# Optimization experiments

Measured on AMD Instinct MI355X. Metric: run time of the kernel, lower is better.

The kernel has to match this reference:

```python
import jax, jax.numpy as jnp
import numpy as np

N = 50000
E = 1600000
IN_CH = 128
HID = 16
HEADS = 8
OUT_CH = 1
NEG_SLOPE = 0.2


def setup_inputs() -> dict:
    key = jax.random.key(0)
    ks = jax.random.split(key, 12)
    x = jax.random.normal(ks[0], (N, IN_CH), dtype=jnp.float32)
    edge_index = jax.random.randint(ks[1], (2, E), 0, N, dtype=jnp.int64)
    s1 = 1.0 / np.sqrt(IN_CH)
    s2 = 1.0 / np.sqrt(HEADS * HID)
    W1 = jax.random.normal(ks[2], (IN_CH, HEADS * HID), dtype=jnp.float32) * s1
    att_src1 = jax.random.normal(ks[3], (HEADS, HID), dtype=jnp.float32) * s1
    att_dst1 = jax.random.normal(ks[4], (HEADS, HID), dtype=jnp.float32) * s1
    b1 = jnp.zeros((HEADS * HID,), dtype=jnp.float32)
    W2 = jax.random.normal(ks[5], (HEADS * HID, OUT_CH), dtype=jnp.float32) * s2
    att_src2 = jax.random.normal(ks[6], (1, OUT_CH), dtype=jnp.float32) * s2
    att_dst2 = jax.random.normal(ks[7], (1, OUT_CH), dtype=jnp.float32) * s2
    b2 = jnp.zeros((OUT_CH,), dtype=jnp.float32)
    return {"x": x, "edge_index": edge_index,
            "W1": W1, "att_src1": att_src1, "att_dst1": att_dst1, "b1": b1,
            "W2": W2, "att_src2": att_src2, "att_dst2": att_dst2, "b2": b2}


def gat_conv(x, src, dst, W, att_src, att_dst, b, heads, concat):
    n = x.shape[0]
    h = (x @ W).reshape(n, heads, -1)               # [N, H, C]
    a_s = jnp.einsum('nhc,hc->nh', h, att_src)      # [N, H]
    a_d = jnp.einsum('nhc,hc->nh', h, att_dst)
    e = jax.nn.leaky_relu(a_s[src] + a_d[dst], NEG_SLOPE)  # [E, H]
    # segment softmax over incoming edges of each dst node
    emax = jax.ops.segment_max(e, dst, num_segments=n)
    p = jnp.exp(e - emax[dst])
    denom = jax.ops.segment_sum(p, dst, num_segments=n)
    alpha = p / (denom[dst] + 1e-16)                 # [E, H]
    msg = h[src] * alpha[:, :, None]                 # [E, H, C]
    out = jax.ops.segment_sum(msg, dst, num_segments=n)  # [N, H, C]
    if concat:
        out = out.reshape(n, -1)
    else:
        out = out.mean(axis=1)
    return out + b


def reference(x, edge_index, W1, att_src1, att_dst1, b1, W2, att_src2, att_dst2, b2):
    n = x.shape[0]
    loops = jnp.arange(n, dtype=edge_index.dtype)
    src = jnp.concatenate([edge_index[0], loops])    # PyG add_self_loops=True
    dst = jnp.concatenate([edge_index[1], loops])
    h = gat_conv(x, src, dst, W1, att_src1, att_dst1, b1, HEADS, True)
    h = jax.nn.elu(h)
    out = gat_conv(h, src, dst, W2, att_src2, att_dst2, b2, 1, False)
    return out
```

## Files before the change

kernel.cpp:

```cpp
#include <hip/hip_runtime.h>
#include <hip/hip_fp16.h>
#include <math.h>

#define N_NODES 50000
#define N_EDGES 1600000
#define NEG 0.2f

#define PB 256
#define CHUNK ((N_EDGES + PB - 1) / PB)
#define BSHIFT 6
#define NBUCK ((N_NODES + 63) >> BSHIFT)
#define LDSE 2816


__global__ __launch_bounds__(1024) void count_pass(const int* __restrict__ ei, int* __restrict__ counts) {
    __shared__ int h[NBUCK];
    for (int i = threadIdx.x; i < NBUCK; i += 1024) h[i] = 0;
    __syncthreads();
    int p = blockIdx.x;
    int e0 = p * CHUNK, e1 = min(e0 + CHUNK, N_EDGES);
    for (int e = e0 + threadIdx.x; e < e1; e += 1024) {
        int d = ei[N_EDGES + e];
        atomicAdd(&h[d >> BSHIFT], 1);
    }
    __syncthreads();
    for (int i = threadIdx.x; i < NBUCK; i += 1024) counts[p * NBUCK + i] = h[i];
}

__global__ __launch_bounds__(256) void scan_blocks(const int* __restrict__ counts,
                                                   int* __restrict__ starts, int* __restrict__ btot) {
    __shared__ int s[256];
    int b = blockIdx.x;
    int t = threadIdx.x;
    int v = counts[t * NBUCK + b];
    s[t] = v;
    __syncthreads();
    for (int off = 1; off < 256; off <<= 1) {
        int u = (t >= off) ? s[t - off] : 0;
        __syncthreads();
        s[t] += u;
        __syncthreads();
    }
    starts[t * NBUCK + b] = s[t] - v;
    if (t == 255) btot[b] = s[255];
}

__global__ __launch_bounds__(1024) void scan_total(const int* __restrict__ btot, int* __restrict__ bbase) {
    __shared__ int s[1024];
    int t = threadIdx.x;
    int v = (t < NBUCK) ? btot[t] : 0;
    s[t] = v;
    __syncthreads();
    for (int off = 1; off < 1024; off <<= 1) {
        int x = (t >= off) ? s[t - off] : 0;
        __syncthreads();
        s[t] += x;
        __syncthreads();
    }
    if (t < NBUCK) bbase[t] = s[t] - v;
    if (t == 0) bbase[NBUCK] = N_EDGES;
}

__global__ __launch_bounds__(1024) void bin_scatter(const int* __restrict__ ei, const int* __restrict__ starts,
                                                    const int* __restrict__ bbase, int* __restrict__ temp) {
    __shared__ int cur[NBUCK];
    int p = blockIdx.x;
    for (int i = threadIdx.x; i < NBUCK; i += 1024)
        cur[i] = bbase[i] + starts[p * NBUCK + i];
    __syncthreads();
    int e0 = p * CHUNK, e1 = min(e0 + CHUNK, N_EDGES);
    for (int e = e0 + threadIdx.x; e < e1; e += 1024) {
        int s = ei[e];
        int d = ei[N_EDGES + e];
        int b = d >> BSHIFT;
        int pos = atomicAdd(&cur[b], 1);
        temp[pos] = s | ((d & 63) << 16);
    }
}


__global__ __launch_bounds__(256) void gemm1_kernel(const float* __restrict__ x, const float* __restrict__ W1,
                                                    const float* __restrict__ att_s, const float* __restrict__ att_d,
                                                    __half2* __restrict__ h1, float* __restrict__ as1,
                                                    float* __restrict__ ad1) {
    __shared__ float xs[128][36];
    int n0 = blockIdx.x * 32;
    int t = threadIdx.x;
#pragma unroll
    for (int i = 0; i < 16; ++i) {
        int f = i * 256 + t;
        int r = f >> 7, c = f & 127;
        int gr = n0 + r;
        float v = (gr < N_NODES) ? x[(size_t)gr * 128 + c] : 0.f;
        xs[c][r] = v;
    }
    __syncthreads();
    int c0 = (t & 31) * 4;
    int r0 = (t >> 5) * 4;
    float acc[4][4];
#pragma unroll
    for (int i = 0; i < 4; ++i)
#pragma unroll
        for (int j = 0; j < 4; ++j) acc[i][j] = 0.f;
#pragma unroll 4
    for (int k = 0; k < 128; ++k) {
        float4 w = *(const float4*)(W1 + k * 128 + c0);
        float4 xr = *(const float4*)(&xs[k][r0]);
        float xv[4] = {xr.x, xr.y, xr.z, xr.w};
        float wv[4] = {w.x, w.y, w.z, w.w};
#pragma unroll
        for (int i = 0; i < 4; ++i)
#pragma unroll
            for (int j = 0; j < 4; ++j) acc[i][j] += xv[i] * wv[j];
    }
#pragma unroll
    for (int i = 0; i < 4; ++i) {
        int row = n0 + r0 + i;
        if (row < N_NODES) {
            __half2 p0 = __float22half2_rn(make_float2(acc[i][0], acc[i][1]));
            __half2 p1 = __float22half2_rn(make_float2(acc[i][2], acc[i][3]));
            h1[(size_t)row * 64 + (c0 >> 1)] = p0;
            h1[(size_t)row * 64 + (c0 >> 1) + 1] = p1;
        }
    }
    int head = (t & 31) >> 2;
    float ps[4], pd[4];
#pragma unroll
    for (int i = 0; i < 4; ++i) {
        float s = 0.f, d = 0.f;
#pragma unroll
        for (int j = 0; j < 4; ++j) {
            s += acc[i][j] * att_s[c0 + j];
            d += acc[i][j] * att_d[c0 + j];
        }
        ps[i] = s; pd[i] = d;
    }
#pragma unroll
    for (int i = 0; i < 4; ++i) {
        ps[i] += __shfl_xor(ps[i], 1, 64);
        ps[i] += __shfl_xor(ps[i], 2, 64);
        pd[i] += __shfl_xor(pd[i], 1, 64);
        pd[i] += __shfl_xor(pd[i], 2, 64);
    }
    if ((t & 3) == 0) {
#pragma unroll
        for (int i = 0; i < 4; ++i) {
            int row = n0 + r0 + i;
            if (row < N_NODES) {
                as1[row * 8 + head] = ps[i];
                ad1[row * 8 + head] = pd[i];
            }
        }
    }
}


__device__ __forceinline__ float lrelu(float v) { return fmaxf(v, NEG * v); }

__global__ __launch_bounds__(512) void agg1_kernel(const char* __restrict__ h1c, const char* __restrict__ as1c,
                                                   const float* __restrict__ ad1, const int* __restrict__ temp,
                                                   const int* __restrict__ bbase, const float* __restrict__ b1,
                                                   const float* __restrict__ W2, float* __restrict__ h2out) {
    __shared__ int lsrc[LDSE];
    __shared__ int cnt[64];
    __shared__ int cur[64];
    __shared__ int lrp[64];
    int b = blockIdx.x, t = threadIdx.x;
    int base = bbase[b];
    int nE = bbase[b + 1] - base;
    if (t < 64) cnt[t] = 0;
    __syncthreads();
    for (int i = t; i < nE; i += 512)
        atomicAdd(&cnt[(unsigned)temp[base + i] >> 16], 1);
    __syncthreads();
    if (t < 64) {
        int v = cnt[t];
        int incl = v;
#pragma unroll
        for (int off = 1; off < 64; off <<= 1) {
            int u = __shfl_up(incl, off, 64);
            if (t >= off) incl += u;
        }
        int excl = incl - v;
        lrp[t] = excl;
        cur[t] = excl;
    }
    __syncthreads();
    for (int i = t; i < nE; i += 512) {
        int v = temp[base + i];
        int pos = atomicAdd(&cur[(unsigned)v >> 16], 1);
        lsrc[pos] = v & 0xFFFF;
    }
    __syncthreads();

    int lane = t & 63;
    int wave = t >> 6;
    int hB = lane >> 3;
    int hP = lane & 7;
    unsigned lane4 = (unsigned)lane << 2;
    unsigned hP4 = (unsigned)hP << 2;
    int bperm_base = hB << 2;
    int prod = lane >> 3;

    for (int kk = 0; kk < 8; ++kk) {
        int k = wave * 8 + kk;
        int n = b * 64 + k;
        if (n >= N_NODES) continue;

        float adP = ad1[n * 8 + hP];
        float adC = ad1[n * 8 + hB];
        float asC = *(const float*)(as1c + ((unsigned)n * 32u + ((unsigned)hB << 2)));
        float p_self = __expf(lrelu(asC + adC));
        __half2 hvs = *(const __half2*)(h1c + (((unsigned)n << 8) + lane4));
        float acc0 = p_self * __half2float(__low2half(hvs));
        float acc1 = p_self * __half2float(__high2half(hvs));
        float l = p_self;

        int jb = lrp[k];
        int deg = cnt[k];
        int j = 0;
        for (; j + 8 <= deg; j += 8) {
            int sP = lsrc[jb + j + prod];
            float aP = *(const float*)(as1c + (((unsigned)sP << 5) + hP4));
            float pP = __expf(lrelu(aP + adP));
            int pPi = __float_as_int(pP);
#pragma unroll
            for (int e = 0; e < 8; ++e) {
                int addr = bperm_base + e * 32;
                float p = __int_as_float(__builtin_amdgcn_ds_bpermute(addr, pPi));
                int s = __builtin_amdgcn_ds_bpermute(addr, sP);
                __half2 hv = *(const __half2*)(h1c + (((unsigned)s << 8) + lane4));
                acc0 += p * __half2float(__low2half(hv));
                acc1 += p * __half2float(__high2half(hv));
                l += p;
            }
        }
        if (j < deg) {
            int r = deg - j;
            int sP = 0;
            float pP = 0.f;
            if (j + prod < deg) {
                sP = lsrc[jb + j + prod];
                float aP = *(const float*)(as1c + (((unsigned)sP << 5) + hP4));
                pP = __expf(lrelu(aP + adP));
            }
            int pPi = __float_as_int(pP);
            for (int e = 0; e < r; ++e) {
                int addr = bperm_base + e * 32;
                float p = __int_as_float(__builtin_amdgcn_ds_bpermute(addr, pPi));
                int s = __builtin_amdgcn_ds_bpermute(addr, sP);
                __half2 hv = *(const __half2*)(h1c + (((unsigned)s << 8) + lane4));
                acc0 += p * __half2float(__low2half(hv));
                acc1 += p * __half2float(__high2half(hv));
                l += p;
            }
        }

        float inv = 1.f / (l + 1e-16f);
        int c0 = lane * 2;
        float y0 = acc0 * inv + b1[c0];
        float y1 = acc1 * inv + b1[c0 + 1];
        y0 = y0 > 0.f ? y0 : expm1f(y0);
        y1 = y1 > 0.f ? y1 : expm1f(y1);
        float part = y0 * W2[c0] + y1 * W2[c0 + 1];
#pragma unroll
        for (int off = 32; off; off >>= 1) part += __shfl_down(part, off, 64);
        if (lane == 0) h2out[n] = part;
    }
}


__global__ __launch_bounds__(256) void agg2_kernel(const float* __restrict__ h2, const int* __restrict__ temp,
                                                   const int* __restrict__ bbase, const float* __restrict__ att_s2,
                                                   const float* __restrict__ att_d2, const float* __restrict__ b2,
                                                   float* __restrict__ out) {
    __shared__ int lsrc[LDSE];
    __shared__ int cnt[64];
    __shared__ int cur[64];
    __shared__ int lrp[64];
    int b = blockIdx.x, t = threadIdx.x;
    int base = bbase[b];
    int nE = bbase[b + 1] - base;
    if (t < 64) cnt[t] = 0;
    __syncthreads();
    for (int i = t; i < nE; i += 256)
        atomicAdd(&cnt[(unsigned)temp[base + i] >> 16], 1);
    __syncthreads();
    if (t < 64) {
        int v = cnt[t];
        int incl = v;
#pragma unroll
        for (int off = 1; off < 64; off <<= 1) {
            int u = __shfl_up(incl, off, 64);
            if (t >= off) incl += u;
        }
        int excl = incl - v;
        lrp[t] = excl;
        cur[t] = excl;
    }
    __syncthreads();
    for (int i = t; i < nE; i += 256) {
        int v = temp[base + i];
        int pos = atomicAdd(&cur[(unsigned)v >> 16], 1);
        lsrc[pos] = v & 0xFFFF;
    }
    __syncthreads();

    float asw = att_s2[0], adw = att_d2[0];
    int lane = t & 63;
    int wave = t >> 6;
    int sub = lane & 7;
    int grp = lane >> 3;
    for (int round = 0; round < 2; ++round) {
        int k = wave * 16 + round * 8 + grp;
        int n = b * 64 + k;
        float acc = 0.f, l = 0.f;
        if (n < N_NODES) {
            float h2n = h2[n];
            float ad = h2n * adw;
            if (sub == 0) {
                float p = __expf(lrelu(h2n * asw + ad));
                acc = p * h2n;
                l = p;
            }
            int jb = lrp[k];
            int deg = cnt[k];
            for (int jj = sub; jj < deg; jj += 8) {
                int s = lsrc[jb + jj];
                float hs = h2[s];
                float p = __expf(lrelu(hs * asw + ad));
                acc += p * hs;
                l += p;
            }
#pragma unroll
            for (int off = 4; off; off >>= 1) {
                acc += __shfl_down(acc, off, 8);
                l += __shfl_down(l, off, 8);
            }
            if (sub == 0) out[n] = acc / (l + 1e-16f) + b2[0];
        }
    }
}


extern "C" void kernel_launch(void* const* d_in, const int* in_sizes, int n_in,
                              void* d_out, int out_size, void* d_ws, size_t ws_size,
                              hipStream_t stream) {
    const float* x = (const float*)d_in[0];
    const int* ei = (const int*)d_in[1];
    const float* W1 = (const float*)d_in[2];
    const float* att_s1 = (const float*)d_in[3];
    const float* att_d1 = (const float*)d_in[4];
    const float* b1 = (const float*)d_in[5];
    const float* W2 = (const float*)d_in[6];
    const float* att_s2 = (const float*)d_in[7];
    const float* att_d2 = (const float*)d_in[8];
    const float* b2 = (const float*)d_in[9];
    float* out = (float*)d_out;

    char* p = (char*)d_ws;
    auto alloc = [&](size_t bytes) {
        char* q = p;
        p += (bytes + 255) & ~(size_t)255;
        return q;
    };
    int* counts = (int*)alloc((size_t)PB * NBUCK * 4);
    int* starts = (int*)alloc((size_t)PB * NBUCK * 4);
    int* btot = (int*)alloc((size_t)NBUCK * 4);
    int* bbase = (int*)alloc((size_t)(NBUCK + 1) * 4);
    int* temp = (int*)alloc((size_t)N_EDGES * 4);
    __half2* h1 = (__half2*)alloc((size_t)N_NODES * 128 * 2);
    float* as1 = (float*)alloc((size_t)N_NODES * 8 * 4);
    float* ad1 = (float*)alloc((size_t)N_NODES * 8 * 4);
    float* h2 = (float*)alloc((size_t)N_NODES * 4);

    count_pass<<<PB, 1024, 0, stream>>>(ei, counts);
    scan_blocks<<<NBUCK, 256, 0, stream>>>(counts, starts, btot);
    scan_total<<<1, 1024, 0, stream>>>(btot, bbase);
    bin_scatter<<<PB, 1024, 0, stream>>>(ei, starts, bbase, temp);
    gemm1_kernel<<<(N_NODES + 31) / 32, 256, 0, stream>>>(x, W1, att_s1, att_d1, h1, as1, ad1);
    agg1_kernel<<<NBUCK, 512, 0, stream>>>((const char*)h1, (const char*)as1, ad1, temp, bbase, b1, W2, h2);
    agg2_kernel<<<NBUCK, 256, 0, stream>>>(h2, temp, bbase, att_s2, att_d2, b2, out);
}
```

Measured before the change: 234.6 us.

## Fuse preprocessing kernels and merge edge scatter with GEMM launch

Bucket totals are now accumulated with global atomics in count_pass, which lets the per-bucket scan and the total scan share a single launch; block NBUCK of that launch scans the bucket totals. The edge binning scatter and the first-layer GEMM are merged into one heterogeneous launch that uses a shared-memory union, so the two independent jobs can run concurrently. agg1 is changed to 256 threads, with each wave handling 16 nodes instead of 8. This cuts the launch count and lets the GEMM overlap the scatter, at the cost of an extra memset and a scatter that now runs with 256-thread blocks instead of 1024.

```diff
diff --git a/kernel.cpp b/kernel.cpp
--- a/kernel.cpp
+++ b/kernel.cpp
@@ -11,9 +11,11 @@
 #define BSHIFT 6
 #define NBUCK ((N_NODES + 63) >> BSHIFT)
 #define LDSE 2816
-
-
-__global__ __launch_bounds__(1024) void count_pass(const int* __restrict__ ei, int* __restrict__ counts) {
+#define GEMMB ((N_NODES + 31) / 32)
+
+
+__global__ __launch_bounds__(1024) void count_pass(const int* __restrict__ ei, int* __restrict__ counts,
+                                                   int* __restrict__ btot) {
     __shared__ int h[NBUCK];
     for (int i = threadIdx.x; i < NBUCK; i += 1024) h[i] = 0;
     __syncthreads();
@@ -24,75 +26,93 @@
         atomicAdd(&h[d >> BSHIFT], 1);
     }
     __syncthreads();
-    for (int i = threadIdx.x; i < NBUCK; i += 1024) counts[p * NBUCK + i] = h[i];
-}
-
-__global__ __launch_bounds__(256) void scan_blocks(const int* __restrict__ counts,
-                                                   int* __restrict__ starts, int* __restrict__ btot) {
+    for (int i = threadIdx.x; i < NBUCK; i += 1024) {
+        counts[p * NBUCK + i] = h[i];
+        if (h[i]) atomicAdd(&btot[i], h[i]);
+    }
+}
+
+
+__global__ __launch_bounds__(256) void scan_fused(const int* __restrict__ counts, const int* __restrict__ btot,
+                                                  int* __restrict__ starts, int* __restrict__ bbase) {
     __shared__ int s[256];
     int b = blockIdx.x;
     int t = threadIdx.x;
-    int v = counts[t * NBUCK + b];
-    s[t] = v;
-    __syncthreads();
-    for (int off = 1; off < 256; off <<= 1) {
-        int u = (t >= off) ? s[t - off] : 0;
+    if (b < NBUCK) {
+        int v = counts[t * NBUCK + b];
+        s[t] = v;
         __syncthreads();
-        s[t] += u;
+        for (int off = 1; off < 256; off <<= 1) {
+            int u = (t >= off) ? s[t - off] : 0;
+            __syncthreads();
+            s[t] += u;
+            __syncthreads();
+        }
+        starts[t * NBUCK + b] = s[t] - v;
+    } else {
+        int base = t * 4;
+        int c[4];
+        int sum = 0;
+#pragma unroll
+        for (int k = 0; k < 4; ++k) {
+            c[k] = (base + k < NBUCK) ? btot[base + k] : 0;
+            sum += c[k];
+        }
+        s[t] = sum;
         __syncthreads();
-    }
-    starts[t * NBUCK + b] = s[t] - v;
-    if (t == 255) btot[b] = s[255];
-}
-
-__global__ __launch_bounds__(1024) void scan_total(const int* __restrict__ btot, int* __restrict__ bbase) {
-    __shared__ int s[1024];
-    int t = threadIdx.x;
-    int v = (t < NBUCK) ? btot[t] : 0;
-    s[t] = v;
-    __syncthreads();
-    for (int off = 1; off < 1024; off <<= 1) {
-        int x = (t >= off) ? s[t - off] : 0;
-        __syncthreads();
-        s[t] += x;
-        __syncthreads();
-    }
-    if (t < NBUCK) bbase[t] = s[t] - v;
-    if (t == 0) bbase[NBUCK] = N_EDGES;
-}
-
-__global__ __launch_bounds__(1024) void bin_scatter(const int* __restrict__ ei, const int* __restrict__ starts,
-                                                    const int* __restrict__ bbase, int* __restrict__ temp) {
-    __shared__ int cur[NBUCK];
-    int p = blockIdx.x;
-    for (int i = threadIdx.x; i < NBUCK; i += 1024)
-        cur[i] = bbase[i] + starts[p * NBUCK + i];
-    __syncthreads();
-    int e0 = p * CHUNK, e1 = min(e0 + CHUNK, N_EDGES);
-    for (int e = e0 + threadIdx.x; e < e1; e += 1024) {
-        int s = ei[e];
-        int d = ei[N_EDGES + e];
-        int b = d >> BSHIFT;
-        int pos = atomicAdd(&cur[b], 1);
-        temp[pos] = s | ((d & 63) << 16);
-    }
-}
-
-
-__global__ __launch_bounds__(256) void gemm1_kernel(const float* __restrict__ x, const float* __restrict__ W1,
+        for (int off = 1; off < 256; off <<= 1) {
+            int u = (t >= off) ? s[t - off] : 0;
+            __syncthreads();
+            s[t] += u;
+            __syncthreads();
+        }
+        int run = s[t] - sum;
+#pragma unroll
+        for (int k = 0; k < 4; ++k) {
+            if (base + k < NBUCK) {
+                bbase[base + k] = run;
+                run += c[k];
+            }
+        }
+        if (t == 0) bbase[NBUCK] = N_EDGES;
+    }
+}
+
+
+__global__ __launch_bounds__(256) void scatter_gemm(const int* __restrict__ ei, const int* __restrict__ starts,
+                                                    const int* __restrict__ bbase, int* __restrict__ temp,
+                                                    const float* __restrict__ x, const float* __restrict__ W1,
                                                     const float* __restrict__ att_s, const float* __restrict__ att_d,
                                                     __half2* __restrict__ h1, float* __restrict__ as1,
                                                     float* __restrict__ ad1) {
-    __shared__ float xs[128][36];
-    int n0 = blockIdx.x * 32;
+    __shared__ union {
+        float xs[128][36];
+        int cur[NBUCK];
+    } u;
     int t = threadIdx.x;
+    if (blockIdx.x < PB) {
+        int p = blockIdx.x;
+        for (int i = t; i < NBUCK; i += 256)
+            u.cur[i] = bbase[i] + starts[p * NBUCK + i];
+        __syncthreads();
+        int e0 = p * CHUNK, e1 = min(e0 + CHUNK, N_EDGES);
+        for (int e = e0 + t; e < e1; e += 256) {
+            int s = ei[e];
+            int d = ei[N_EDGES + e];
+            int b = d >> BSHIFT;
+            int pos = atomicAdd(&u.cur[b], 1);
+            temp[pos] = s | ((d & 63) << 16);
+        }
+        return;
+    }
+    int n0 = (blockIdx.x - PB) * 32;
 #pragma unroll
     for (int i = 0; i < 16; ++i) {
         int f = i * 256 + t;
         int r = f >> 7, c = f & 127;
         int gr = n0 + r;
         float v = (gr < N_NODES) ? x[(size_t)gr * 128 + c] : 0.f;
-        xs[c][r] = v;
+        u.xs[c][r] = v;
     }
     __syncthreads();
     int c0 = (t & 31) * 4;
@@ -105,7 +125,7 @@
 #pragma unroll 4
     for (int k = 0; k < 128; ++k) {
         float4 w = *(const float4*)(W1 + k * 128 + c0);
-        float4 xr = *(const float4*)(&xs[k][r0]);
+        float4 xr = *(const float4*)(&u.xs[k][r0]);
         float xv[4] = {xr.x, xr.y, xr.z, xr.w};
         float wv[4] = {w.x, w.y, w.z, w.w};
 #pragma unroll
@@ -157,7 +177,7 @@
 
 __device__ __forceinline__ float lrelu(float v) { return fmaxf(v, NEG * v); }
 
-__global__ __launch_bounds__(512) void agg1_kernel(const char* __restrict__ h1c, const char* __restrict__ as1c,
+__global__ __launch_bounds__(256) void agg1_kernel(const char* __restrict__ h1c, const char* __restrict__ as1c,
                                                    const float* __restrict__ ad1, const int* __restrict__ temp,
                                                    const int* __restrict__ bbase, const float* __restrict__ b1,
                                                    const float* __restrict__ W2, float* __restrict__ h2out) {
@@ -170,7 +190,7 @@
     int nE = bbase[b + 1] - base;
     if (t < 64) cnt[t] = 0;
     __syncthreads();
-    for (int i = t; i < nE; i += 512)
+    for (int i = t; i < nE; i += 256)
         atomicAdd(&cnt[(unsigned)temp[base + i] >> 16], 1);
     __syncthreads();
     if (t < 64) {
@@ -186,7 +206,7 @@
         cur[t] = excl;
     }
     __syncthreads();
-    for (int i = t; i < nE; i += 512) {
+    for (int i = t; i < nE; i += 256) {
         int v = temp[base + i];
         int pos = atomicAdd(&cur[(unsigned)v >> 16], 1);
         lsrc[pos] = v & 0xFFFF;
@@ -202,8 +222,8 @@
     int bperm_base = hB << 2;
     int prod = lane >> 3;
 
-    for (int kk = 0; kk < 8; ++kk) {
-        int k = wave * 8 + kk;
+    for (int kk = 0; kk < 16; ++kk) {
+        int k = wave * 16 + kk;
         int n = b * 64 + k;
         if (n >= N_NODES) continue;
 
@@ -374,11 +394,11 @@
     float* ad1 = (float*)alloc((size_t)N_NODES * 8 * 4);
     float* h2 = (float*)alloc((size_t)N_NODES * 4);
 
-    count_pass<<<PB, 1024, 0, stream>>>(ei, counts);
-    scan_blocks<<<NBUCK, 256, 0, stream>>>(counts, starts, btot);
-    scan_total<<<1, 1024, 0, stream>>>(btot, bbase);
-    bin_scatter<<<PB, 1024, 0, stream>>>(ei, starts, bbase, temp);
-    gemm1_kernel<<<(N_NODES + 31) / 32, 256, 0, stream>>>(x, W1, att_s1, att_d1, h1, as1, ad1);
-    agg1_kernel<<<NBUCK, 512, 0, stream>>>((const char*)h1, (const char*)as1, ad1, temp, bbase, b1, W2, h2);
+    hipMemsetAsync(btot, 0, (size_t)NBUCK * 4, stream);
+    count_pass<<<PB, 1024, 0, stream>>>(ei, counts, btot);
+    scan_fused<<<NBUCK + 1, 256, 0, stream>>>(counts, btot, starts, bbase);
+    scatter_gemm<<<PB + GEMMB, 256, 0, stream>>>(ei, starts, bbase, temp,
+                                                 x, W1, att_s1, att_d1, h1, as1, ad1);
+    agg1_kernel<<<NBUCK, 256, 0, stream>>>((const char*)h1, (const char*)as1, ad1, temp, bbase, b1, W2, h2);
     agg2_kernel<<<NBUCK, 256, 0, stream>>>(h2, temp, bbase, att_s2, att_d2, b2, out);
 }
```

Measured after the change: 258.6 us. 10.2% more time.

## Fuse bin scatter with GEMM launch and shrink buckets to 32 nodes

Applied to the files above, without the earlier changes.

Merges the edge bin-scatter and the first-layer GEMM into one launch, where the first PB blocks do the scatter and the rest do the GEMM. The two independent phases can then overlap and one launch is removed. Bucket size also drops from 64 to 32 nodes, which doubles the number of aggregation blocks and halves their thread count and LDS use. scan_total now handles two buckets per thread to cover the larger bucket count. The risk is an LDS overflow in a high-degree bucket (LDSE is 1536) and more atomics and count overhead from the extra buckets.

```diff
diff --git a/kernel.cpp b/kernel.cpp
--- a/kernel.cpp
+++ b/kernel.cpp
@@ -8,9 +8,10 @@
 
 #define PB 256
 #define CHUNK ((N_EDGES + PB - 1) / PB)
-#define BSHIFT 6
-#define NBUCK ((N_NODES + 63) >> BSHIFT)
-#define LDSE 2816
+#define BSHIFT 5
+#define NBUCK ((N_NODES + 31) >> BSHIFT)
+#define LDSE 1536
+#define GEMMB ((N_NODES + 31) / 32)
 
 
 __global__ __launch_bounds__(1024) void count_pass(const int* __restrict__ ei, int* __restrict__ counts) {
@@ -26,6 +27,7 @@
     __syncthreads();
     for (int i = threadIdx.x; i < NBUCK; i += 1024) counts[p * NBUCK + i] = h[i];
 }
+
 
 __global__ __launch_bounds__(256) void scan_blocks(const int* __restrict__ counts,
                                                    int* __restrict__ starts, int* __restrict__ btot) {
@@ -48,8 +50,11 @@
 __global__ __launch_bounds__(1024) void scan_total(const int* __restrict__ btot, int* __restrict__ bbase) {
     __shared__ int s[1024];
     int t = threadIdx.x;
-    int v = (t < NBUCK) ? btot[t] : 0;
-    s[t] = v;
+    int base = t * 2;
+    int c0 = (base < NBUCK) ? btot[base] : 0;
+    int c1 = (base + 1 < NBUCK) ? btot[base + 1] : 0;
+    int sum = c0 + c1;
+    s[t] = sum;
     __syncthreads();
     for (int off = 1; off < 1024; off <<= 1) {
         int x = (t >= off) ? s[t - off] : 0;
@@ -57,42 +62,47 @@
         s[t] += x;
         __syncthreads();
     }
-    if (t < NBUCK) bbase[t] = s[t] - v;
+    int run = s[t] - sum;
+    if (base < NBUCK) bbase[base] = run;
+    if (base + 1 < NBUCK) bbase[base + 1] = run + c0;
     if (t == 0) bbase[NBUCK] = N_EDGES;
 }
 
-__global__ __launch_bounds__(1024) void bin_scatter(const int* __restrict__ ei, const int* __restrict__ starts,
-                                                    const int* __restrict__ bbase, int* __restrict__ temp) {
-    __shared__ int cur[NBUCK];
-    int p = blockIdx.x;
-    for (int i = threadIdx.x; i < NBUCK; i += 1024)
-        cur[i] = bbase[i] + starts[p * NBUCK + i];
-    __syncthreads();
-    int e0 = p * CHUNK, e1 = min(e0 + CHUNK, N_EDGES);
-    for (int e = e0 + threadIdx.x; e < e1; e += 1024) {
-        int s = ei[e];
-        int d = ei[N_EDGES + e];
-        int b = d >> BSHIFT;
-        int pos = atomicAdd(&cur[b], 1);
-        temp[pos] = s | ((d & 63) << 16);
-    }
-}
-
-
-__global__ __launch_bounds__(256) void gemm1_kernel(const float* __restrict__ x, const float* __restrict__ W1,
+
+__global__ __launch_bounds__(256) void scatter_gemm(const int* __restrict__ ei, const int* __restrict__ starts,
+                                                    const int* __restrict__ bbase, int* __restrict__ temp,
+                                                    const float* __restrict__ x, const float* __restrict__ W1,
                                                     const float* __restrict__ att_s, const float* __restrict__ att_d,
                                                     __half2* __restrict__ h1, float* __restrict__ as1,
                                                     float* __restrict__ ad1) {
-    __shared__ float xs[128][36];
-    int n0 = blockIdx.x * 32;
+    __shared__ union {
+        float xs[128][36];
+        int cur[NBUCK];
+    } u;
     int t = threadIdx.x;
+    if (blockIdx.x < PB) {
+        int p = blockIdx.x;
+        for (int i = t; i < NBUCK; i += 256)
+            u.cur[i] = bbase[i] + starts[p * NBUCK + i];
+        __syncthreads();
+        int e0 = p * CHUNK, e1 = min(e0 + CHUNK, N_EDGES);
+        for (int e = e0 + t; e < e1; e += 256) {
+            int s = ei[e];
+            int d = ei[N_EDGES + e];
+            int b = d >> BSHIFT;
+            int pos = atomicAdd(&u.cur[b], 1);
+            temp[pos] = s | ((d & 31) << 16);
+        }
+        return;
+    }
+    int n0 = (blockIdx.x - PB) * 32;
 #pragma unroll
     for (int i = 0; i < 16; ++i) {
         int f = i * 256 + t;
         int r = f >> 7, c = f & 127;
         int gr = n0 + r;
         float v = (gr < N_NODES) ? x[(size_t)gr * 128 + c] : 0.f;
-        xs[c][r] = v;
+        u.xs[c][r] = v;
     }
     __syncthreads();
     int c0 = (t & 31) * 4;
@@ -105,7 +115,7 @@
 #pragma unroll 4
     for (int k = 0; k < 128; ++k) {
         float4 w = *(const float4*)(W1 + k * 128 + c0);
-        float4 xr = *(const float4*)(&xs[k][r0]);
+        float4 xr = *(const float4*)(&u.xs[k][r0]);
         float xv[4] = {xr.x, xr.y, xr.z, xr.w};
         float wv[4] = {w.x, w.y, w.z, w.w};
 #pragma unroll
@@ -157,28 +167,28 @@
 
 __device__ __forceinline__ float lrelu(float v) { return fmaxf(v, NEG * v); }
 
-__global__ __launch_bounds__(512) void agg1_kernel(const char* __restrict__ h1c, const char* __restrict__ as1c,
+__global__ __launch_bounds__(256) void agg1_kernel(const char* __restrict__ h1c, const char* __restrict__ as1c,
                                                    const float* __restrict__ ad1, const int* __restrict__ temp,
                                                    const int* __restrict__ bbase, const float* __restrict__ b1,
                                                    const float* __restrict__ W2, float* __restrict__ h2out) {
     __shared__ int lsrc[LDSE];
-    __shared__ int cnt[64];
-    __shared__ int cur[64];
-    __shared__ int lrp[64];
+    __shared__ int cnt[32];
+    __shared__ int cur[32];
+    __shared__ int lrp[32];
     int b = blockIdx.x, t = threadIdx.x;
     int base = bbase[b];
     int nE = bbase[b + 1] - base;
-    if (t < 64) cnt[t] = 0;
-    __syncthreads();
-    for (int i = t; i < nE; i += 512)
+    if (t < 32) cnt[t] = 0;
+    __syncthreads();
+    for (int i = t; i < nE; i += 256)
         atomicAdd(&cnt[(unsigned)temp[base + i] >> 16], 1);
     __syncthreads();
-    if (t < 64) {
+    if (t < 32) {
         int v = cnt[t];
         int incl = v;
 #pragma unroll
-        for (int off = 1; off < 64; off <<= 1) {
-            int u = __shfl_up(incl, off, 64);
+        for (int off = 1; off < 32; off <<= 1) {
+            int u = __shfl_up(incl, off, 32);
             if (t >= off) incl += u;
         }
         int excl = incl - v;
@@ -186,7 +196,7 @@
         cur[t] = excl;
     }
     __syncthreads();
-    for (int i = t; i < nE; i += 512) {
+    for (int i = t; i < nE; i += 256) {
         int v = temp[base + i];
         int pos = atomicAdd(&cur[(unsigned)v >> 16], 1);
         lsrc[pos] = v & 0xFFFF;
@@ -204,7 +214,7 @@
 
     for (int kk = 0; kk < 8; ++kk) {
         int k = wave * 8 + kk;
-        int n = b * 64 + k;
+        int n = b * 32 + k;
         if (n >= N_NODES) continue;
 
         float adP = ad1[n * 8 + hP];
@@ -275,23 +285,23 @@
                                                    const float* __restrict__ att_d2, const float* __restrict__ b2,
                                                    float* __restrict__ out) {
     __shared__ int lsrc[LDSE];
-    __shared__ int cnt[64];
-    __shared__ int cur[64];
-    __shared__ int lrp[64];
+    __shared__ int cnt[32];
+    __shared__ int cur[32];
+    __shared__ int lrp[32];
     int b = blockIdx.x, t = threadIdx.x;
     int base = bbase[b];
     int nE = bbase[b + 1] - base;
-    if (t < 64) cnt[t] = 0;
+    if (t < 32) cnt[t] = 0;
     __syncthreads();
     for (int i = t; i < nE; i += 256)
         atomicAdd(&cnt[(unsigned)temp[base + i] >> 16], 1);
     __syncthreads();
-    if (t < 64) {
+    if (t < 32) {
         int v = cnt[t];
         int incl = v;
 #pragma unroll
-        for (int off = 1; off < 64; off <<= 1) {
-            int u = __shfl_up(incl, off, 64);
+        for (int off = 1; off < 32; off <<= 1) {
+            int u = __shfl_up(incl, off, 32);
             if (t >= off) incl += u;
         }
         int excl = incl - v;
@@ -311,34 +321,32 @@
     int wave = t >> 6;
     int sub = lane & 7;
     int grp = lane >> 3;
-    for (int round = 0; round < 2; ++round) {
-        int k = wave * 16 + round * 8 + grp;
-        int n = b * 64 + k;
+    int k = wave * 8 + grp;
+    int n = b * 32 + k;
+    if (n < N_NODES) {
+        float h2n = h2[n];
+        float ad = h2n * adw;
         float acc = 0.f, l = 0.f;
-        if (n < N_NODES) {
-            float h2n = h2[n];
-            float ad = h2n * adw;
-            if (sub == 0) {
-                float p = __expf(lrelu(h2n * asw + ad));
-                acc = p * h2n;
-                l = p;
-            }
-            int jb = lrp[k];
-            int deg = cnt[k];
-            for (int jj = sub; jj < deg; jj += 8) {
-                int s = lsrc[jb + jj];
-                float hs = h2[s];
-                float p = __expf(lrelu(hs * asw + ad));
-                acc += p * hs;
-                l += p;
-            }
-#pragma unroll
-            for (int off = 4; off; off >>= 1) {
-                acc += __shfl_down(acc, off, 8);
-                l += __shfl_down(l, off, 8);
-            }
-            if (sub == 0) out[n] = acc / (l + 1e-16f) + b2[0];
-        }
+        if (sub == 0) {
+            float p = __expf(lrelu(h2n * asw + ad));
+            acc = p * h2n;
+            l = p;
+        }
+        int jb = lrp[k];
+        int deg = cnt[k];
+        for (int jj = sub; jj < deg; jj += 8) {
+            int s = lsrc[jb + jj];
+            float hs = h2[s];
+            float p = __expf(lrelu(hs * asw + ad));
+            acc += p * hs;
+            l += p;
+        }
+#pragma unroll
+        for (int off = 4; off; off >>= 1) {
+            acc += __shfl_down(acc, off, 8);
+            l += __shfl_down(l, off, 8);
+        }
+        if (sub == 0) out[n] = acc / (l + 1e-16f) + b2[0];
     }
 }
 
@@ -377,8 +385,8 @@
     count_pass<<<PB, 1024, 0, stream>>>(ei, counts);
     scan_blocks<<<NBUCK, 256, 0, stream>>>(counts, starts, btot);
     scan_total<<<1, 1024, 0, stream>>>(btot, bbase);
-    bin_scatter<<<PB, 1024, 0, stream>>>(ei, starts, bbase, temp);
-    gemm1_kernel<<<(N_NODES + 31) / 32, 256, 0, stream>>>(x, W1, att_s1, att_d1, h1, as1, ad1);
-    agg1_kernel<<<NBUCK, 512, 0, stream>>>((const char*)h1, (const char*)as1, ad1, temp, bbase, b1, W2, h2);
+    scatter_gemm<<<PB + GEMMB, 256, 0, stream>>>(ei, starts, bbase, temp,
+                                                 x, W1, att_s1, att_d1, h1, as1, ad1);
+    agg1_kernel<<<NBUCK, 256, 0, stream>>>((const char*)h1, (const char*)as1, ad1, temp, bbase, b1, W2, h2);
     agg2_kernel<<<NBUCK, 256, 0, stream>>>(h2, temp, bbase, att_s2, att_d2, b2, out);
 }
```

New measurement: 230.0 us. -2.0%, faster.
